# Performance work log

Hardware: AMD Instinct MI355X
Metric: run time of the kernel (lower is better)

The kernel has to match this reference:

```python
import jax, jax.numpy as jnp
import numpy as np

H, IN, D, RD, A = 1024, 14, 100000, 10, 2

def setup_inputs() -> dict:
    key = jax.random.key(0)
    ks = jax.random.split(key, 12)
    f = lambda k, shp, s=1.0: jax.random.normal(k, shp, dtype=jnp.float32) * s
    return {
        "x_t": f(ks[0], (1, IN)),
        "h": f(ks[1], (1, 1, H), 0.1),
        "c": f(ks[2], (1, 1, H), 0.1),
        "keys": f(ks[3], (D, RD)),
        "vals": f(ks[4], (D, H)),
        "W_i2h": f(ks[5], (5 * H, IN), 0.1),
        "b_i2h": jnp.zeros((5 * H,), jnp.float32),
        "W_h2h": f(ks[6], (5 * H, H), 0.03),
        "b_h2h": jnp.zeros((5 * H,), jnp.float32),
        "W_ih": f(ks[7], (H, H), 0.03),
        "b_ih": jnp.zeros((H,), jnp.float32),
        "W_actor": f(ks[8], (A, H), 0.03),
        "b_actor": jnp.zeros((A,), jnp.float32),
        "W_critic": f(ks[9], (1, H), 0.03),
        "b_critic": jnp.zeros((1,), jnp.float32),
        "pick_arm": 0,
    }


def reference(x_t, h, c, keys, vals, W_i2h, b_i2h, W_h2h, b_h2h,
              W_ih, b_ih, W_actor, b_actor, W_critic, b_critic, pick_arm):
    Hd = W_h2h.shape[1]
    Rd = keys.shape[1]
    h2 = h.reshape(h.shape[1], -1)   # [1, H]
    c2 = c.reshape(c.shape[1], -1)   # [1, H]
    # fused i2h + h2h preactivation: [1, 5H]
    preact = x_t @ W_i2h.T + b_i2h + h2 @ W_h2h.T + b_h2h
    gates = jax.nn.sigmoid(preact[:, :4 * Hd])
    f_t = gates[:, :Hd]
    i_t = gates[:, Hd:2 * Hd]
    o_t = gates[:, 2 * Hd:3 * Hd]
    r_t = gates[:, 3 * Hd:4 * Hd]
    c_new = jnp.tanh(preact[:, 4 * Hd:])
    c_t = f_t * c2 + i_t * c_new
    # DND read: cosine similarity over stored keys, softmax-weighted value sum
    q = jax.lax.dynamic_slice(x_t[0], (pick_arm * Rd,), (Rd,))  # retrieval key
    dots = keys @ q                                              # [D]
    denom = jnp.maximum(jnp.linalg.norm(keys, axis=1) * jnp.linalg.norm(q), 1e-8)
    w = jax.nn.softmax(dots / denom)                             # [D]
    m_t = jnp.tanh(w @ vals)                                     # [H]
    c_t = c_t + r_t * m_t
    h_t = o_t * jnp.tanh(c_t)
    # A2C head (standard dnd-lstm A2C): shared relu layer, actor softmax, critic scalar
    hh = jax.nn.relu(h_t @ W_ih.T + b_ih)
    pi = jax.nn.softmax(hh @ W_actor.T + b_actor, axis=-1)       # [1, A]
    v = hh @ W_critic.T + b_critic                               # [1, 1]
    # categorical sampling with a fixed key (replaces torch.distributions sample)
    a = jax.random.categorical(jax.random.key(1), jnp.log(pi[0]))
    logp = jnp.log(pi[0, a])
    # pack: [pi(A), v(1), log_prob(1), h_t(H), c_t(H)]
    return jnp.concatenate([pi[0], v[0], logp[None], h_t[0], c_t[0]])
```

## Files before the change

### kernel.cpp

```cpp
#include <hip/hip_runtime.h>
#include <math.h>

#define NHID 1024
#define NIN 14
#define NKEYS 100000
#define NRD 10
#define R3 50
#define NB3 2000
#define NBPRE 1280
#define NSLOT 8

typedef float f32x4 __attribute__((ext_vector_type(4)));

#define WS_MACC8   0
#define WS_L8      8192
#define WS_PREACT  8208
#define WS_HH      13328
#define WS_HT      14352
#define ZERO_BYTES ((8192 + NSLOT) * 4)

__device__ inline float wave_reduce_sum(float v) {
#pragma unroll
    for (int off = 32; off > 0; off >>= 1) v += __shfl_down(v, off, 64);
    return v;
}

__device__ inline float sigm(float x) { return 1.0f / (1.0f + expf(-x)); }

__device__ inline float load_q(const float* __restrict__ x, int pick, float* q) {
    int start = pick * NRD;
    if (start > NIN - NRD) start = NIN - NRD;
    if (start < 0) start = 0;
    float qn = 0.f;
#pragma unroll
    for (int k = 0; k < NRD; ++k) { q[k] = x[start + k]; qn = fmaf(q[k], q[k], qn); }
    return sqrtf(qn);
}

__device__ inline float score_for(const float* __restrict__ keys, int i,
                                  const float* q, float qn) {
    float dot = 0.f, kn = 0.f;
#pragma unroll
    for (int k = 0; k < NRD; ++k) {
        float kv = keys[(size_t)i * NRD + k];
        dot = fmaf(kv, q[k], dot);
        kn = fmaf(kv, kv, kn);
    }
    return dot / fmaxf(sqrtf(kn) * qn, 1e-8f);
}

__global__ void __launch_bounds__(256) kA(const float* __restrict__ keys,
                                          const float* __restrict__ x,
                                          const int* __restrict__ pick_arm,
                                          const float* __restrict__ vals,
                                          float* __restrict__ macc8,
                                          float* __restrict__ L8,
                                          const float* __restrict__ h,
                                          const float* __restrict__ Wi,
                                          const float* __restrict__ bi,
                                          const float* __restrict__ Wh,
                                          const float* __restrict__ bh,
                                          float* __restrict__ preact) {
    int tid = threadIdx.x;
    if (blockIdx.x < NB3) {
        __shared__ float wl[R3];
        int r0 = blockIdx.x * R3;
        int slot = blockIdx.x & (NSLOT - 1);
        float wv = 0.f;
        if (tid < R3) {
            float q[NRD];
            float qn = load_q(x, pick_arm[0], q);
            float sv = score_for(keys, r0 + tid, q, qn);
            wv = expf(sv);
            wl[tid] = wv;
        }
        if (tid < 64) {
            float ls = wave_reduce_sum(wv);
            if (tid == 0) atomicAdd(&L8[slot], ls);
        }
        __syncthreads();
        const f32x4* vp = (const f32x4*)vals + ((size_t)r0 << 8) + tid;
        float ax = 0.f, ay = 0.f, az = 0.f, aw = 0.f;
#pragma unroll 5
        for (int r = 0; r < R3; ++r) {
            float w = wl[r];
            f32x4 v = __builtin_nontemporal_load(&vp[(size_t)r << 8]);
            ax = fmaf(w, v.x, ax);
            ay = fmaf(w, v.y, ay);
            az = fmaf(w, v.z, az);
            aw = fmaf(w, v.w, aw);
        }
        float* ms = macc8 + (size_t)slot * NHID;
        atomicAdd(&ms[4 * tid + 0], ax);
        atomicAdd(&ms[4 * tid + 1], ay);
        atomicAdd(&ms[4 * tid + 2], az);
        atomicAdd(&ms[4 * tid + 3], aw);
    } else {
        int wave = tid >> 6, lane = tid & 63;
        int row = (blockIdx.x - NB3) * 4 + wave;
        const float4* w4 = (const float4*)(Wh + (size_t)row * NHID);
        const float4* h4 = (const float4*)h;
        float p = 0.f;
#pragma unroll
        for (int j = 0; j < 4; ++j) {
            float4 wv = w4[j * 64 + lane];
            float4 hv = h4[j * 64 + lane];
            p += wv.x * hv.x + wv.y * hv.y + wv.z * hv.z + wv.w * hv.w;
        }
        if (lane < NIN) p += x[lane] * Wi[(size_t)row * NIN + lane];
        p = wave_reduce_sum(p);
        if (lane == 0) preact[row] = p + bi[row] + bh[row];
    }
}

__global__ void k4_cell(const float* __restrict__ preact, const float* __restrict__ macc8,
                        const float* __restrict__ L8, const float* __restrict__ c_in,
                        float* __restrict__ out, float* __restrict__ ht_ws) {
    int t = blockIdx.x * 256 + threadIdx.x;
    float Ls = 0.f, msum = 0.f;
#pragma unroll
    for (int s = 0; s < NSLOT; ++s) {
        Ls += L8[s];
        msum += macc8[(size_t)s * NHID + t];
    }
    float f = sigm(preact[t]);
    float i = sigm(preact[NHID + t]);
    float o = sigm(preact[2 * NHID + t]);
    float r = sigm(preact[3 * NHID + t]);
    float cn = tanhf(preact[4 * NHID + t]);
    float mt = tanhf(msum / Ls);
    float ct = f * c_in[t] + i * cn + r * mt;
    float ht = o * tanhf(ct);
    out[4 + t] = ht;
    out[4 + NHID + t] = ct;
    ht_ws[t] = ht;
}

__global__ void k5_hh(const float* __restrict__ ht, const float* __restrict__ Wih,
                      const float* __restrict__ bih, float* __restrict__ hh) {
    int wave = threadIdx.x >> 6, lane = threadIdx.x & 63;
    int row = blockIdx.x * 4 + wave;
    const float4* w4 = (const float4*)(Wih + (size_t)row * NHID);
    const float4* h4 = (const float4*)ht;
    float p = 0.f;
#pragma unroll
    for (int j = 0; j < 4; ++j) {
        float4 wv = w4[j * 64 + lane];
        float4 hv = h4[j * 64 + lane];
        p += wv.x * hv.x + wv.y * hv.y + wv.z * hv.z + wv.w * hv.w;
    }
    p = wave_reduce_sum(p);
    if (lane == 0) hh[row] = fmaxf(p + bih[row], 0.f);
}

#define TF_ROUND(r) { x0 += x1; x1 = (x1 << r) | (x1 >> (32 - r)); x1 ^= x0; }

__global__ void k6_heads(const float* __restrict__ hh, const float* __restrict__ Wa,
                         const float* __restrict__ ba, const float* __restrict__ Wc,
                         const float* __restrict__ bc, float* __restrict__ out) {
    __shared__ float zz[3];
    int wave = threadIdx.x >> 6, lane = threadIdx.x & 63;
    if (wave < 3) {
        const float* W = (wave == 2) ? Wc : Wa + wave * NHID;
        const float4* w4 = (const float4*)W;
        const float4* h4 = (const float4*)hh;
        float p = 0.f;
#pragma unroll
        for (int j = 0; j < 4; ++j) {
            float4 wv = w4[j * 64 + lane];
            float4 hv = h4[j * 64 + lane];
            p += wv.x * hv.x + wv.y * hv.y + wv.z * hv.z + wv.w * hv.w;
        }
        p = wave_reduce_sum(p);
        if (lane == 0) zz[wave] = p;
    }
    __syncthreads();
    if (threadIdx.x == 0) {
        float z0 = zz[0] + ba[0], z1 = zz[1] + ba[1], v = zz[2] + bc[0];
        float mz = fmaxf(z0, z1);
        float e0 = expf(z0 - mz), e1 = expf(z1 - mz);
        float sum = e0 + e1;
        float pi0 = e0 / sum, pi1 = e1 / sum;
        float lse = mz + logf(sum);
        unsigned ks0 = 0u, ks1 = 1u, ks2 = 0u ^ 1u ^ 0x1BD11BDAu;
        unsigned x0 = 0u + ks0, x1 = 1u + ks1;
        TF_ROUND(13) TF_ROUND(15) TF_ROUND(26) TF_ROUND(6)
        x0 += ks1; x1 += ks2 + 1u;
        TF_ROUND(17) TF_ROUND(29) TF_ROUND(16) TF_ROUND(24)
        x0 += ks2; x1 += ks0 + 2u;
        TF_ROUND(13) TF_ROUND(15) TF_ROUND(26) TF_ROUND(6)
        x0 += ks0; x1 += ks1 + 3u;
        TF_ROUND(17) TF_ROUND(29) TF_ROUND(16) TF_ROUND(24)
        x0 += ks1; x1 += ks2 + 4u;
        TF_ROUND(13) TF_ROUND(15) TF_ROUND(26) TF_ROUND(6)
        x0 += ks2; x1 += ks0 + 5u;
        float u0 = __uint_as_float((x0 >> 9) | 0x3F800000u) - 1.0f;
        float u1 = __uint_as_float((x1 >> 9) | 0x3F800000u) - 1.0f;
        const float tiny = 1.17549435e-38f;
        u0 = fmaxf(u0, tiny); u1 = fmaxf(u1, tiny);
        float g0 = -logf(-logf(u0));
        float g1 = -logf(-logf(u1));
        int a = (z1 + g1 > z0 + g0) ? 1 : 0;
        float logp = (a ? z1 : z0) - lse;
        out[0] = pi0; out[1] = pi1; out[2] = v; out[3] = logp;
    }
}

extern "C" void kernel_launch(void* const* d_in, const int* in_sizes, int n_in,
                              void* d_out, int out_size, void* d_ws, size_t ws_size,
                              hipStream_t stream) {
    const float* x      = (const float*)d_in[0];
    const float* h      = (const float*)d_in[1];
    const float* c      = (const float*)d_in[2];
    const float* keys   = (const float*)d_in[3];
    const float* vals   = (const float*)d_in[4];
    const float* Wi2h   = (const float*)d_in[5];
    const float* bi2h   = (const float*)d_in[6];
    const float* Wh2h   = (const float*)d_in[7];
    const float* bh2h   = (const float*)d_in[8];
    const float* Wih    = (const float*)d_in[9];
    const float* bih    = (const float*)d_in[10];
    const float* Wact   = (const float*)d_in[11];
    const float* bact   = (const float*)d_in[12];
    const float* Wcrit  = (const float*)d_in[13];
    const float* bcrit  = (const float*)d_in[14];
    const int*   pick   = (const int*)d_in[15];
    float* out = (float*)d_out;
    float* ws  = (float*)d_ws;

    (void)hipMemsetAsync(ws, 0, ZERO_BYTES, stream);
    kA<<<NB3 + NBPRE, 256, 0, stream>>>(keys, x, pick, vals,
                                        ws + WS_MACC8, ws + WS_L8,
                                        h, Wi2h, bi2h, Wh2h, bh2h, ws + WS_PREACT);
    k4_cell<<<4, 256, 0, stream>>>(ws + WS_PREACT, ws + WS_MACC8, ws + WS_L8,
                                   c, out, ws + WS_HT);
    k5_hh<<<NHID / 4, 256, 0, stream>>>(ws + WS_HT, Wih, bih, ws + WS_HH);
    k6_heads<<<1, 256, 0, stream>>>(ws + WS_HH, Wact, bact, Wcrit, bcrit, out);
}
```

Measured before the change: 110.6 us.

## Fuse LSTM cell update into hidden-layer GEMV kernel and widen atomic slots

Merges the cell-update kernel into the W_ih GEMV kernel: every block recomputes the full h_t into shared memory, so one launch and a global round trip are removed. The number of atomic accumulation slots doubles from 8 to 16 to reduce contention on the DND value accumulation. It also adds nontemporal loads for the weight matrices and raises the unroll factor of the vals loop. The cost is 256 blocks each redundantly reading preact, macc and c and evaluating the transcendentals, and k45 now sums twice as many slots.

```diff
diff --git a/kernel.cpp b/kernel.cpp
--- a/kernel.cpp
+++ b/kernel.cpp
@@ -8,16 +8,15 @@
 #define R3 50
 #define NB3 2000
 #define NBPRE 1280
-#define NSLOT 8
+#define NSLOT 16
 
 typedef float f32x4 __attribute__((ext_vector_type(4)));
 
-#define WS_MACC8   0
-#define WS_L8      8192
-#define WS_PREACT  8208
-#define WS_HH      13328
-#define WS_HT      14352
-#define ZERO_BYTES ((8192 + NSLOT) * 4)
+#define WS_MACC    0
+#define WS_L       16384
+#define WS_PREACT  16400
+#define WS_HH      21520
+#define ZERO_BYTES ((16384 + NSLOT) * 4)
 
 __device__ inline float wave_reduce_sum(float v) {
 #pragma unroll
@@ -53,8 +52,8 @@
                                           const float* __restrict__ x,
                                           const int* __restrict__ pick_arm,
                                           const float* __restrict__ vals,
-                                          float* __restrict__ macc8,
-                                          float* __restrict__ L8,
+                                          float* __restrict__ macc,
+                                          float* __restrict__ Lacc,
                                           const float* __restrict__ h,
                                           const float* __restrict__ Wi,
                                           const float* __restrict__ bi,
@@ -76,12 +75,12 @@
         }
         if (tid < 64) {
             float ls = wave_reduce_sum(wv);
-            if (tid == 0) atomicAdd(&L8[slot], ls);
+            if (tid == 0) atomicAdd(&Lacc[slot], ls);
         }
         __syncthreads();
         const f32x4* vp = (const f32x4*)vals + ((size_t)r0 << 8) + tid;
         float ax = 0.f, ay = 0.f, az = 0.f, aw = 0.f;
-#pragma unroll 5
+#pragma unroll 10
         for (int r = 0; r < R3; ++r) {
             float w = wl[r];
             f32x4 v = __builtin_nontemporal_load(&vp[(size_t)r << 8]);
@@ -90,7 +89,7 @@
             az = fmaf(w, v.z, az);
             aw = fmaf(w, v.w, aw);
         }
-        float* ms = macc8 + (size_t)slot * NHID;
+        float* ms = macc + (size_t)slot * NHID;
         atomicAdd(&ms[4 * tid + 0], ax);
         atomicAdd(&ms[4 * tid + 1], ay);
         atomicAdd(&ms[4 * tid + 2], az);
@@ -98,13 +97,13 @@
     } else {
         int wave = tid >> 6, lane = tid & 63;
         int row = (blockIdx.x - NB3) * 4 + wave;
-        const float4* w4 = (const float4*)(Wh + (size_t)row * NHID);
-        const float4* h4 = (const float4*)h;
+        const f32x4* w4 = (const f32x4*)(Wh + (size_t)row * NHID);
+        const f32x4* h4 = (const f32x4*)h;
         float p = 0.f;
 #pragma unroll
         for (int j = 0; j < 4; ++j) {
-            float4 wv = w4[j * 64 + lane];
-            float4 hv = h4[j * 64 + lane];
+            f32x4 wv = __builtin_nontemporal_load(&w4[j * 64 + lane]);
+            f32x4 hv = h4[j * 64 + lane];
             p += wv.x * hv.x + wv.y * hv.y + wv.z * hv.z + wv.w * hv.w;
         }
         if (lane < NIN) p += x[lane] * Wi[(size_t)row * NIN + lane];
@@ -113,40 +112,58 @@
     }
 }
 
-__global__ void k4_cell(const float* __restrict__ preact, const float* __restrict__ macc8,
-                        const float* __restrict__ L8, const float* __restrict__ c_in,
-                        float* __restrict__ out, float* __restrict__ ht_ws) {
-    int t = blockIdx.x * 256 + threadIdx.x;
-    float Ls = 0.f, msum = 0.f;
-#pragma unroll
-    for (int s = 0; s < NSLOT; ++s) {
-        Ls += L8[s];
-        msum += macc8[(size_t)s * NHID + t];
-    }
-    float f = sigm(preact[t]);
-    float i = sigm(preact[NHID + t]);
-    float o = sigm(preact[2 * NHID + t]);
-    float r = sigm(preact[3 * NHID + t]);
-    float cn = tanhf(preact[4 * NHID + t]);
-    float mt = tanhf(msum / Ls);
-    float ct = f * c_in[t] + i * cn + r * mt;
-    float ht = o * tanhf(ct);
-    out[4 + t] = ht;
-    out[4 + NHID + t] = ct;
-    ht_ws[t] = ht;
-}
-
-__global__ void k5_hh(const float* __restrict__ ht, const float* __restrict__ Wih,
-                      const float* __restrict__ bih, float* __restrict__ hh) {
-    int wave = threadIdx.x >> 6, lane = threadIdx.x & 63;
+__global__ void __launch_bounds__(256) k45(const float* __restrict__ preact,
+                                           const float* __restrict__ macc,
+                                           const float* __restrict__ Lacc,
+                                           const float* __restrict__ c_in,
+                                           const float* __restrict__ Wih,
+                                           const float* __restrict__ bih,
+                                           float* __restrict__ out,
+                                           float* __restrict__ hh) {
+    __shared__ float hlds[NHID];
+    int tid = threadIdx.x;
+    float Ls = 0.f;
+#pragma unroll
+    for (int s = 0; s < NSLOT; ++s) Ls += Lacc[s];
+    float invL = 1.0f / Ls;
+    const f32x4* pre4 = (const f32x4*)preact;
+    f32x4 fg = pre4[tid];
+    f32x4 ig = pre4[256 + tid];
+    f32x4 og = pre4[512 + tid];
+    f32x4 rg = pre4[768 + tid];
+    f32x4 gg = pre4[1024 + tid];
+    f32x4 m4 = {0.f, 0.f, 0.f, 0.f};
+#pragma unroll
+    for (int s = 0; s < NSLOT; ++s) m4 += ((const f32x4*)(macc + (size_t)s * NHID))[tid];
+    f32x4 c4 = ((const f32x4*)c_in)[tid];
+    f32x4 h4, ct4;
+#pragma unroll
+    for (int e = 0; e < 4; ++e) {
+        float f = sigm(fg[e]);
+        float i = sigm(ig[e]);
+        float o = sigm(og[e]);
+        float r = sigm(rg[e]);
+        float cn = tanhf(gg[e]);
+        float mt = tanhf(m4[e] * invL);
+        float ct = f * c4[e] + i * cn + r * mt;
+        ct4[e] = ct;
+        h4[e] = o * tanhf(ct);
+    }
+    ((f32x4*)hlds)[tid] = h4;
+    if (blockIdx.x == 0) {
+        ((f32x4*)(out + 4))[tid] = h4;
+        ((f32x4*)(out + 4 + NHID))[tid] = ct4;
+    }
+    __syncthreads();
+    int wave = tid >> 6, lane = tid & 63;
     int row = blockIdx.x * 4 + wave;
-    const float4* w4 = (const float4*)(Wih + (size_t)row * NHID);
-    const float4* h4 = (const float4*)ht;
+    const f32x4* w4 = (const f32x4*)(Wih + (size_t)row * NHID);
+    const f32x4* hl4 = (const f32x4*)hlds;
     float p = 0.f;
 #pragma unroll
     for (int j = 0; j < 4; ++j) {
-        float4 wv = w4[j * 64 + lane];
-        float4 hv = h4[j * 64 + lane];
+        f32x4 wv = __builtin_nontemporal_load(&w4[j * 64 + lane]);
+        f32x4 hv = hl4[j * 64 + lane];
         p += wv.x * hv.x + wv.y * hv.y + wv.z * hv.z + wv.w * hv.w;
     }
     p = wave_reduce_sum(p);
@@ -162,13 +179,13 @@
     int wave = threadIdx.x >> 6, lane = threadIdx.x & 63;
     if (wave < 3) {
         const float* W = (wave == 2) ? Wc : Wa + wave * NHID;
-        const float4* w4 = (const float4*)W;
-        const float4* h4 = (const float4*)hh;
+        const f32x4* w4 = (const f32x4*)W;
+        const f32x4* h4 = (const f32x4*)hh;
         float p = 0.f;
 #pragma unroll
         for (int j = 0; j < 4; ++j) {
-            float4 wv = w4[j * 64 + lane];
-            float4 hv = h4[j * 64 + lane];
+            f32x4 wv = w4[j * 64 + lane];
+            f32x4 hv = h4[j * 64 + lane];
             p += wv.x * hv.x + wv.y * hv.y + wv.z * hv.z + wv.w * hv.w;
         }
         p = wave_reduce_sum(p);
@@ -230,10 +247,9 @@
 
     (void)hipMemsetAsync(ws, 0, ZERO_BYTES, stream);
     kA<<<NB3 + NBPRE, 256, 0, stream>>>(keys, x, pick, vals,
-                                        ws + WS_MACC8, ws + WS_L8,
+                                        ws + WS_MACC, ws + WS_L,
                                         h, Wi2h, bi2h, Wh2h, bh2h, ws + WS_PREACT);
-    k4_cell<<<4, 256, 0, stream>>>(ws + WS_PREACT, ws + WS_MACC8, ws + WS_L8,
-                                   c, out, ws + WS_HT);
-    k5_hh<<<NHID / 4, 256, 0, stream>>>(ws + WS_HT, Wih, bih, ws + WS_HH);
+    k45<<<NHID / 4, 256, 0, stream>>>(ws + WS_PREACT, ws + WS_MACC, ws + WS_L,
+                                      c, Wih, bih, out, ws + WS_HH);
     k6_heads<<<1, 256, 0, stream>>>(ws + WS_HH, Wact, bact, Wcrit, bcrit, out);
 }
```

Result: faster. 107.9 us (-2.5%).
